# Kernel tuning notes

Hardware: AMD Instinct MI355X
Metric: run time of the kernel (lower is better)

Reference implementation:

```python
import jax, jax.numpy as jnp
import numpy as np

B = 2048          # batch
K = 32            # max active features per side
NF = 22528        # feature_set.num_features
L1 = 2048
L2 = 16
L3 = 32
P = 8             # num_psqt_buckets
NLS = 8           # num_ls_buckets
QP = 255.0        # 8-bit unsigned LSQ upper bound


def setup_inputs() -> dict:
    key = jax.random.key(0)
    ks = jax.random.split(key, 16)
    us = jax.random.bernoulli(ks[0], 0.5, (B, 1)).astype(jnp.float32)
    them = 1.0 - us
    white_indices = jax.random.randint(ks[1], (B, K), 0, NF)
    black_indices = jax.random.randint(ks[2], (B, K), 0, NF)
    white_values = jnp.ones((B, K), jnp.float32)
    black_values = jnp.ones((B, K), jnp.float32)
    psqt_indices = jax.random.randint(ks[3], (B,), 0, P)
    layer_stack_indices = jax.random.randint(ks[4], (B,), 0, NLS)
    # parameters
    ft_weight = jax.random.normal(ks[5], (NF, L1 + P), jnp.float32) * 0.01
    ft_bias = jax.random.normal(ks[6], (L1 + P,), jnp.float32) * 0.01
    lsq_s = jnp.full((4,), 1.0 / 128.0, jnp.float32)  # per-group step size
    W1 = jax.random.normal(ks[7], (NLS, L2, L1), jnp.float32) * (1.0 / np.sqrt(L1))
    b1 = jnp.zeros((NLS, L2), jnp.float32)
    W2 = jax.random.normal(ks[8], (NLS, L3, L2), jnp.float32) * (1.0 / np.sqrt(L2))
    b2 = jnp.zeros((NLS, L3), jnp.float32)
    Wo = jax.random.normal(ks[9], (NLS, 1, L3), jnp.float32) * (1.0 / np.sqrt(L3))
    bo = jnp.zeros((NLS, 1), jnp.float32)
    return dict(us=us, them=them, white_indices=white_indices, white_values=white_values,
                black_indices=black_indices, black_values=black_values,
                psqt_indices=psqt_indices, layer_stack_indices=layer_stack_indices,
                ft_weight=ft_weight, ft_bias=ft_bias, lsq_s=lsq_s,
                W1=W1, b1=b1, W2=W2, b2=b2, Wo=Wo, bo=bo)


def _feature_transform(idx, val, ft_weight, ft_bias):
    # sparse accumulation: sum_k val[b,k] * ft_weight[idx[b,k], :]
    emb = ft_weight[idx]                           # [B, K, L1+P]
    return jnp.einsum('bk,bkd->bd', val, emb) + ft_bias


def _lsq(x, s):
    # LSQ activation, 4 groups over feature dim, 8-bit unsigned, STE round
    b, d = x.shape
    g = x.reshape(b, 4, d // 4) / s[None, :, None]
    gc = jnp.clip(g, 0.0, QP)
    gq = gc + jax.lax.stop_gradient(jnp.round(gc) - gc)
    return (gq * s[None, :, None]).reshape(b, d)


def reference(us, them, white_indices, white_values, black_indices, black_values,
              psqt_indices, layer_stack_indices,
              ft_weight, ft_bias, lsq_s, W1, b1, W2, b2, Wo, bo):
    wp = _feature_transform(white_indices, white_values, ft_weight, ft_bias)
    bp = _feature_transform(black_indices, black_values, ft_weight, ft_bias)
    w, wpsqt = wp[:, :L1], wp[:, L1:]
    b, bpsqt = bp[:, :L1], bp[:, L1:]
    l0 = us * jnp.concatenate([w, b], axis=1) + them * jnp.concatenate([b, w], axis=1)
    l0q = _lsq(l0, lsq_s)                          # [B, 2*L1]
    s0, s1, s2, s3 = jnp.split(l0q, 4, axis=1)
    l0_mixed = jnp.concatenate([s0 * s1, s2 * s3], axis=1)   # [B, L1]
    # psqt bucket gather
    wps = jnp.take_along_axis(wpsqt, psqt_indices[:, None], axis=1)  # [B,1]
    bps = jnp.take_along_axis(bpsqt, psqt_indices[:, None], axis=1)
    # per-sample layer-stack (expert) selection
    i = layer_stack_indices
    h1 = jnp.clip(jnp.einsum('bi,boi->bo', l0_mixed, W1[i]) + b1[i], 0.0, 1.0)
    h2 = jnp.clip(jnp.einsum('bi,boi->bo', h1, W2[i]) + b2[i], 0.0, 1.0)
    ls_out = jnp.einsum('bi,boi->bo', h2, Wo[i]) + bo[i]     # [B,1]
    return ls_out + (wps - bps) * (us - 0.5)
```

## Files before the change

### kernel.cpp

```cpp
#include <hip/hip_runtime.h>

#define BB 2048
#define K 32
#define ROW 2056
#define L1D 2048
#define NT 512

__device__ __forceinline__ void fma4(float4& a, float v, const float4 t) {
    a.x = fmaf(v, t.x, a.x); a.y = fmaf(v, t.y, a.y);
    a.z = fmaf(v, t.z, a.z); a.w = fmaf(v, t.w, a.w);
}

__device__ __forceinline__ float4 add4(float4 a, float4 b) {
    float4 r; r.x = a.x + b.x; r.y = a.y + b.y; r.z = a.z + b.z; r.w = a.w + b.w;
    return r;
}

__device__ __forceinline__ float4 mix4(float ua, float4 a, float ub, float4 b) {
    float4 r;
    r.x = fmaf(ua, a.x, ub * b.x); r.y = fmaf(ua, a.y, ub * b.y);
    r.z = fmaf(ua, a.z, ub * b.z); r.w = fmaf(ua, a.w, ub * b.w);
    return r;
}

__device__ __forceinline__ float lsq1(float g, float s) {
    return rintf(fminf(fmaxf(g / s, 0.f), 255.f)) * s;
}

__device__ __forceinline__ float4 lsq4(float4 g, float s) {
    float4 r;
    r.x = lsq1(g.x, s); r.y = lsq1(g.y, s); r.z = lsq1(g.z, s); r.w = lsq1(g.w, s);
    return r;
}

__device__ __forceinline__ float4 mul4(float4 a, float4 b) {
    float4 r; r.x = a.x * b.x; r.y = a.y * b.y; r.z = a.z * b.z; r.w = a.w * b.w;
    return r;
}

__global__ __launch_bounds__(NT, 8) void nnue_fwd(
    const float* __restrict__ us_p,
    const float* __restrict__ them_p,
    const int*   __restrict__ widx,
    const float* __restrict__ wval,
    const int*   __restrict__ bidx,
    const float* __restrict__ bval,
    const int*   __restrict__ psqt_idx,
    const int*   __restrict__ ls_idx,
    const float* __restrict__ ftw,
    const float* __restrict__ ftb,
    const float* __restrict__ lsq_s,
    const float* __restrict__ W1,
    const float* __restrict__ b1,
    const float* __restrict__ W2,
    const float* __restrict__ b2,
    const float* __restrict__ Wo,
    const float* __restrict__ bo,
    float* __restrict__ out)
{
    const int b = blockIdx.x;
    const int t = threadIdx.x;

    __shared__ float4 sQA[NT];
    __shared__ float4 sQB[NT];
    __shared__ float4 sM[NT];
    __shared__ float  sH1t[16];
    __shared__ float  sH1[16];
    __shared__ float  sH2[32];
    __shared__ float  sPsq;

    const float usv = us_p[b];
    const float thv = them_p[b];

    float4 aw = {0,0,0,0}, ab = {0,0,0,0};
    #pragma unroll 4
    for (int k = 0; k < K; ++k) {
        const int   iw = widx[b * K + k];
        const float vw = wval[b * K + k];
        const int   ib = bidx[b * K + k];
        const float vb = bval[b * K + k];
        const float4* rw = (const float4*)(ftw + (size_t)iw * ROW);
        const float4* rb = (const float4*)(ftw + (size_t)ib * ROW);
        fma4(aw, vw, rw[t]);
        fma4(ab, vb, rb[t]);
    }

    const int pi = psqt_idx[b];
    if (t < 64) {
        const int k = t & 31;
        const int   idx = (t < 32) ? widx[b * K + k] : bidx[b * K + k];
        const float val = (t < 32) ? wval[b * K + k] : bval[b * K + k];
        float c = val * ftw[(size_t)idx * ROW + 2048 + pi];
        c += __shfl_down(c, 16, 32); c += __shfl_down(c, 8, 32);
        c += __shfl_down(c, 4, 32);  c += __shfl_down(c, 2, 32);
        c += __shfl_down(c, 1, 32);
        const float bsum = __shfl(c, 32);
        if (t == 0) sPsq = (c - bsum) * (usv - 0.5f);
    }

    const float s0 = lsq_s[0], s1 = lsq_s[1], s2 = lsq_s[2], s3 = lsq_s[3];
    const float4 bias = ((const float4*)ftb)[t];
    aw = add4(aw, bias);
    ab = add4(ab, bias);
    const float sA = (t < 256) ? s0 : s1;
    const float sB = (t < 256) ? s2 : s3;
    sQA[t] = lsq4(mix4(usv, aw, thv, ab), sA);
    sQB[t] = lsq4(mix4(usv, ab, thv, aw), sB);
    __syncthreads();

    if (t < 256) {
        sM[t]       = mul4(sQA[t], sQA[t + 256]);
        sM[t + 256] = mul4(sQB[t], sQB[t + 256]);
    }
    __syncthreads();

    const int i = ls_idx[b];
    const float* W1i = W1 + (size_t)i * 16 * L1D;
    {
        const int o   = t >> 5;
        const int sub = t & 31;
        const float4* Wrow = (const float4*)(W1i + o * L1D);
        float4 a4 = {0,0,0,0};
        #pragma unroll
        for (int jj = 0; jj < 16; ++jj) {
            const int j4 = sub + (jj << 5);
            const float4 m = sM[j4];
            const float4 w = Wrow[j4];
            a4.x = fmaf(m.x, w.x, a4.x); a4.y = fmaf(m.y, w.y, a4.y);
            a4.z = fmaf(m.z, w.z, a4.z); a4.w = fmaf(m.w, w.w, a4.w);
        }
        float acc = (a4.x + a4.y) + (a4.z + a4.w);
        acc += __shfl_down(acc, 16, 32); acc += __shfl_down(acc, 8, 32);
        acc += __shfl_down(acc, 4, 32);  acc += __shfl_down(acc, 2, 32);
        acc += __shfl_down(acc, 1, 32);
        if (sub == 0) sH1t[o] = acc;
    }
    __syncthreads();

    if (t < 16) {
        const float v = sH1t[t] + b1[i * 16 + t];
        sH1[t] = fminf(fmaxf(v, 0.f), 1.f);
    }
    __syncthreads();

    if (t < 32) {
        const float* W2i = W2 + (size_t)i * 32 * 16 + t * 16;
        float v = b2[i * 32 + t];
        #pragma unroll
        for (int j = 0; j < 16; ++j) v = fmaf(sH1[j], W2i[j], v);
        sH2[t] = fminf(fmaxf(v, 0.f), 1.f);
    }
    __syncthreads();

    if (t == 0) {
        const float* Woi = Wo + (size_t)i * 32;
        float v = bo[i];
        #pragma unroll
        for (int j = 0; j < 32; ++j) v = fmaf(sH2[j], Woi[j], v);
        out[b] = v + sPsq;
    }
}

extern "C" void kernel_launch(void* const* d_in, const int* in_sizes, int n_in,
                              void* d_out, int out_size, void* d_ws, size_t ws_size,
                              hipStream_t stream) {
    const float* us_p  = (const float*)d_in[0];
    const float* them  = (const float*)d_in[1];
    const int*   widx  = (const int*)d_in[2];
    const float* wval  = (const float*)d_in[3];
    const int*   bidx  = (const int*)d_in[4];
    const float* bval  = (const float*)d_in[5];
    const int*   pidx  = (const int*)d_in[6];
    const int*   lidx  = (const int*)d_in[7];
    const float* ftw   = (const float*)d_in[8];
    const float* ftb   = (const float*)d_in[9];
    const float* lsqs  = (const float*)d_in[10];
    const float* W1    = (const float*)d_in[11];
    const float* b1    = (const float*)d_in[12];
    const float* W2    = (const float*)d_in[13];
    const float* b2    = (const float*)d_in[14];
    const float* Wo    = (const float*)d_in[15];
    const float* bo    = (const float*)d_in[16];
    float* out = (float*)d_out;

    nnue_fwd<<<dim3(BB), dim3(NT), 0, stream>>>(
        us_p, them, widx, wval, bidx, bval, pidx, lidx,
        ftw, ftb, lsqs, W1, b1, W2, b2, Wo, bo, out);
}
```

Baseline: 396.5 us.

## Convert feature table and W1 to bf16 in workspace before gather

```diff
diff --git a/kernel.cpp b/kernel.cpp
--- a/kernel.cpp
+++ b/kernel.cpp
@@ -5,10 +5,31 @@
 #define ROW 2056
 #define L1D 2048
 #define NT 512
+#define NFEAT 22528
+#define TBL_ELEMS ((size_t)NFEAT * ROW)
+#define W1_ELEMS  ((size_t)8 * 16 * L1D)
+#define TBL_BYTES (TBL_ELEMS * 2)
+#define W1_OFF    TBL_BYTES
+#define WS_NEEDED (TBL_BYTES + W1_ELEMS * 2)
+
+__device__ __forceinline__ float bf2f(unsigned short s) {
+    union { unsigned int u; float f; } v; v.u = ((unsigned int)s) << 16; return v.f;
+}
+
+__device__ __forceinline__ unsigned short f2bf(float f) {
+    union { float f; unsigned int u; } v; v.f = f;
+    const unsigned int u = v.u;
+    return (unsigned short)((u + 0x7fffu + ((u >> 16) & 1u)) >> 16);
+}
 
 __device__ __forceinline__ void fma4(float4& a, float v, const float4 t) {
     a.x = fmaf(v, t.x, a.x); a.y = fmaf(v, t.y, a.y);
     a.z = fmaf(v, t.z, a.z); a.w = fmaf(v, t.w, a.w);
+}
+
+__device__ __forceinline__ void fma4u(float4& a, float v, const ushort4 t) {
+    a.x = fmaf(v, bf2f(t.x), a.x); a.y = fmaf(v, bf2f(t.y), a.y);
+    a.z = fmaf(v, bf2f(t.z), a.z); a.w = fmaf(v, bf2f(t.w), a.w);
 }
 
 __device__ __forceinline__ float4 add4(float4 a, float4 b) {
@@ -38,7 +59,20 @@
     return r;
 }
 
-__global__ __launch_bounds__(NT, 8) void nnue_fwd(
+__global__ __launch_bounds__(256) void conv_bf16(const float* __restrict__ src,
+                                                 unsigned short* __restrict__ dst,
+                                                 int n4) {
+    int i = blockIdx.x * 256 + threadIdx.x;
+    const int stride = gridDim.x * 256;
+    for (; i < n4; i += stride) {
+        const float4 v = ((const float4*)src)[i];
+        ushort4 o;
+        o.x = f2bf(v.x); o.y = f2bf(v.y); o.z = f2bf(v.z); o.w = f2bf(v.w);
+        ((ushort4*)dst)[i] = o;
+    }
+}
+
+__global__ __launch_bounds__(NT, 8) void nnue_fwd_bf16(
     const float* __restrict__ us_p,
     const float* __restrict__ them_p,
     const int*   __restrict__ widx,
@@ -47,10 +81,10 @@
     const float* __restrict__ bval,
     const int*   __restrict__ psqt_idx,
     const int*   __restrict__ ls_idx,
-    const float* __restrict__ ftw,
+    const unsigned short* __restrict__ tbl,
     const float* __restrict__ ftb,
     const float* __restrict__ lsq_s,
-    const float* __restrict__ W1,
+    const unsigned short* __restrict__ w1bf,
     const float* __restrict__ b1,
     const float* __restrict__ W2,
     const float* __restrict__ b2,
@@ -79,10 +113,10 @@
         const float vw = wval[b * K + k];
         const int   ib = bidx[b * K + k];
         const float vb = bval[b * K + k];
-        const float4* rw = (const float4*)(ftw + (size_t)iw * ROW);
-        const float4* rb = (const float4*)(ftw + (size_t)ib * ROW);
-        fma4(aw, vw, rw[t]);
-        fma4(ab, vb, rb[t]);
+        const ushort4 uw = ((const ushort4*)(tbl + (size_t)iw * ROW))[t];
+        const ushort4 ub = ((const ushort4*)(tbl + (size_t)ib * ROW))[t];
+        fma4u(aw, vw, uw);
+        fma4u(ab, vb, ub);
     }
 
     const int pi = psqt_idx[b];
@@ -90,7 +124,7 @@
         const int k = t & 31;
         const int   idx = (t < 32) ? widx[b * K + k] : bidx[b * K + k];
         const float val = (t < 32) ? wval[b * K + k] : bval[b * K + k];
-        float c = val * ftw[(size_t)idx * ROW + 2048 + pi];
+        float c = val * bf2f(tbl[(size_t)idx * ROW + 2048 + pi]);
         c += __shfl_down(c, 16, 32); c += __shfl_down(c, 8, 32);
         c += __shfl_down(c, 4, 32);  c += __shfl_down(c, 2, 32);
         c += __shfl_down(c, 1, 32);
@@ -115,19 +149,19 @@
     __syncthreads();
 
     const int i = ls_idx[b];
-    const float* W1i = W1 + (size_t)i * 16 * L1D;
+    const unsigned short* W1i = w1bf + (size_t)i * 16 * L1D;
     {
         const int o   = t >> 5;
         const int sub = t & 31;
-        const float4* Wrow = (const float4*)(W1i + o * L1D);
+        const ushort4* Wrow = (const ushort4*)(W1i + o * L1D);
         float4 a4 = {0,0,0,0};
         #pragma unroll
         for (int jj = 0; jj < 16; ++jj) {
             const int j4 = sub + (jj << 5);
-            const float4 m = sM[j4];
-            const float4 w = Wrow[j4];
-            a4.x = fmaf(m.x, w.x, a4.x); a4.y = fmaf(m.y, w.y, a4.y);
-            a4.z = fmaf(m.z, w.z, a4.z); a4.w = fmaf(m.w, w.w, a4.w);
+            const float4  m = sM[j4];
+            const ushort4 w = Wrow[j4];
+            a4.x = fmaf(m.x, bf2f(w.x), a4.x); a4.y = fmaf(m.y, bf2f(w.y), a4.y);
+            a4.z = fmaf(m.z, bf2f(w.z), a4.z); a4.w = fmaf(m.w, bf2f(w.w), a4.w);
         }
         float acc = (a4.x + a4.y) + (a4.z + a4.w);
         acc += __shfl_down(acc, 16, 32); acc += __shfl_down(acc, 8, 32);
@@ -152,6 +186,90 @@
     }
     __syncthreads();
 
+    if (t == 0) {
+        const float* Woi = Wo + (size_t)i * 32;
+        float v = bo[i];
+        #pragma unroll
+        for (int j = 0; j < 32; ++j) v = fmaf(sH2[j], Woi[j], v);
+        out[b] = v + sPsq;
+    }
+}
+
+__global__ __launch_bounds__(NT, 8) void nnue_fwd_f32(
+    const float* __restrict__ us_p, const float* __restrict__ them_p,
+    const int* __restrict__ widx, const float* __restrict__ wval,
+    const int* __restrict__ bidx, const float* __restrict__ bval,
+    const int* __restrict__ psqt_idx, const int* __restrict__ ls_idx,
+    const float* __restrict__ ftw, const float* __restrict__ ftb,
+    const float* __restrict__ lsq_s, const float* __restrict__ W1,
+    const float* __restrict__ b1, const float* __restrict__ W2,
+    const float* __restrict__ b2, const float* __restrict__ Wo,
+    const float* __restrict__ bo, float* __restrict__ out)
+{
+    const int b = blockIdx.x;
+    const int t = threadIdx.x;
+    __shared__ float4 sQA[NT]; __shared__ float4 sQB[NT]; __shared__ float4 sM[NT];
+    __shared__ float sH1t[16]; __shared__ float sH1[16]; __shared__ float sH2[32];
+    __shared__ float sPsq;
+    const float usv = us_p[b]; const float thv = them_p[b];
+    float4 aw = {0,0,0,0}, ab = {0,0,0,0};
+    #pragma unroll 4
+    for (int k = 0; k < K; ++k) {
+        const int iw = widx[b*K+k]; const float vw = wval[b*K+k];
+        const int ib = bidx[b*K+k]; const float vb = bval[b*K+k];
+        fma4(aw, vw, ((const float4*)(ftw + (size_t)iw * ROW))[t]);
+        fma4(ab, vb, ((const float4*)(ftw + (size_t)ib * ROW))[t]);
+    }
+    const int pi = psqt_idx[b];
+    if (t < 64) {
+        const int k = t & 31;
+        const int   idx = (t < 32) ? widx[b*K+k] : bidx[b*K+k];
+        const float val = (t < 32) ? wval[b*K+k] : bval[b*K+k];
+        float c = val * ftw[(size_t)idx * ROW + 2048 + pi];
+        c += __shfl_down(c, 16, 32); c += __shfl_down(c, 8, 32);
+        c += __shfl_down(c, 4, 32); c += __shfl_down(c, 2, 32); c += __shfl_down(c, 1, 32);
+        const float bsum = __shfl(c, 32);
+        if (t == 0) sPsq = (c - bsum) * (usv - 0.5f);
+    }
+    const float s0 = lsq_s[0], s1 = lsq_s[1], s2 = lsq_s[2], s3 = lsq_s[3];
+    const float4 bias = ((const float4*)ftb)[t];
+    aw = add4(aw, bias); ab = add4(ab, bias);
+    const float sA = (t < 256) ? s0 : s1;
+    const float sB = (t < 256) ? s2 : s3;
+    sQA[t] = lsq4(mix4(usv, aw, thv, ab), sA);
+    sQB[t] = lsq4(mix4(usv, ab, thv, aw), sB);
+    __syncthreads();
+    if (t < 256) { sM[t] = mul4(sQA[t], sQA[t+256]); sM[t+256] = mul4(sQB[t], sQB[t+256]); }
+    __syncthreads();
+    const int i = ls_idx[b];
+    const float* W1i = W1 + (size_t)i * 16 * L1D;
+    {
+        const int o = t >> 5; const int sub = t & 31;
+        const float4* Wrow = (const float4*)(W1i + o * L1D);
+        float4 a4 = {0,0,0,0};
+        #pragma unroll
+        for (int jj = 0; jj < 16; ++jj) {
+            const int j4 = sub + (jj << 5);
+            const float4 m = sM[j4]; const float4 w = Wrow[j4];
+            a4.x = fmaf(m.x, w.x, a4.x); a4.y = fmaf(m.y, w.y, a4.y);
+            a4.z = fmaf(m.z, w.z, a4.z); a4.w = fmaf(m.w, w.w, a4.w);
+        }
+        float acc = (a4.x + a4.y) + (a4.z + a4.w);
+        acc += __shfl_down(acc, 16, 32); acc += __shfl_down(acc, 8, 32);
+        acc += __shfl_down(acc, 4, 32); acc += __shfl_down(acc, 2, 32); acc += __shfl_down(acc, 1, 32);
+        if (sub == 0) sH1t[o] = acc;
+    }
+    __syncthreads();
+    if (t < 16) sH1[t] = fminf(fmaxf(sH1t[t] + b1[i*16+t], 0.f), 1.f);
+    __syncthreads();
+    if (t < 32) {
+        const float* W2i = W2 + (size_t)i * 32 * 16 + t * 16;
+        float v = b2[i*32+t];
+        #pragma unroll
+        for (int j = 0; j < 16; ++j) v = fmaf(sH1[j], W2i[j], v);
+        sH2[t] = fminf(fmaxf(v, 0.f), 1.f);
+    }
+    __syncthreads();
     if (t == 0) {
         const float* Woi = Wo + (size_t)i * 32;
         float v = bo[i];
@@ -183,7 +301,17 @@
     const float* bo    = (const float*)d_in[16];
     float* out = (float*)d_out;
 
-    nnue_fwd<<<dim3(BB), dim3(NT), 0, stream>>>(
-        us_p, them, widx, wval, bidx, bval, pidx, lidx,
-        ftw, ftb, lsqs, W1, b1, W2, b2, Wo, bo, out);
-}
+    if (ws_size >= WS_NEEDED) {
+        unsigned short* tblbf = (unsigned short*)d_ws;
+        unsigned short* w1bf  = (unsigned short*)((char*)d_ws + W1_OFF);
+        conv_bf16<<<dim3(8192), dim3(256), 0, stream>>>(ftw, tblbf, (int)(TBL_ELEMS / 4));
+        conv_bf16<<<dim3(256),  dim3(256), 0, stream>>>(W1,  w1bf,  (int)(W1_ELEMS / 4));
+        nnue_fwd_bf16<<<dim3(BB), dim3(NT), 0, stream>>>(
+            us_p, them, widx, wval, bidx, bval, pidx, lidx,
+            tblbf, ftb, lsqs, w1bf, b1, W2, b2, Wo, bo, out);
+    } else {
+        nnue_fwd_f32<<<dim3(BB), dim3(NT), 0, stream>>>(
+            us_p, them, widx, wval, bidx, bval, pidx, lidx,
+            ftw, ftb, lsqs, W1, b1, W2, b2, Wo, bo, out);
+    }
+}
```

Result: faster. 371.5 us (-6.3%).
